# Performance work log

Hardware: AMD Instinct MI355X
Metric: run time of the kernel (lower is better)

## Reference

```python
import jax, jax.numpy as jnp
import numpy as np

EPS = 1e-6

def _complex_linear(xr, xi, wr, wi):
    # torch Linear: y = x @ W.T ; complex: (xr+i*xi)(Wr+i*Wi)
    yr = jnp.einsum('bsd,ed->bse', xr, wr) - jnp.einsum('bsd,ed->bse', xi, wi)
    yi = jnp.einsum('bsd,ed->bse', xr, wi) + jnp.einsum('bsd,ed->bse', xi, wr)
    return yr, yi

def setup_inputs() -> dict:
    key = jax.random.key(0)
    ks = jax.random.split(key, 12)
    B, S, D = 32768, 16, 64
    inp = {
        'z_real': jax.random.normal(ks[0], (B, D), jnp.float32),
        'z_imag': jax.random.normal(ks[1], (B, D), jnp.float32),
        'mem':    jax.random.normal(ks[2], (B, S, 2 * D), jnp.float32),
        'ptr':    jax.random.uniform(ks[3], (B, S), jnp.float32),
        'ctrl':   jax.random.normal(ks[4], (B, 3), jnp.float32),
        'wq_r': jax.random.normal(ks[5], (D, D), jnp.float32) / np.sqrt(D),
        'wq_i': jax.random.normal(ks[6], (D, D), jnp.float32) / np.sqrt(D),
        'wk_r': jax.random.normal(ks[7], (D, D), jnp.float32) / np.sqrt(D),
        'wk_i': jax.random.normal(ks[8], (D, D), jnp.float32) / np.sqrt(D),
        'wv_r': jax.random.normal(ks[9], (D, D), jnp.float32) / np.sqrt(D),
        'wv_i': jax.random.normal(ks[10], (D, D), jnp.float32) / np.sqrt(D),
    }
    return inp

def reference(z_real, z_imag, mem, ptr, ctrl, wq_r, wq_i, wk_r, wk_i, wv_r, wv_i):
    D = z_real.shape[-1]
    # soft push/pop/stay gates, normalized
    g = jax.nn.sigmoid(ctrl)  # (B,3)
    push, pop, stay = g[:, 0:1], g[:, 1:2], g[:, 2:3]
    total = push + pop + stay + EPS
    push, pop, stay = push / total, pop / total, stay / total
    # pointer update via rolls
    ptr_up = jnp.roll(ptr, 1, axis=1)
    ptr_down = jnp.roll(ptr, -1, axis=1)
    new_ptr = push * ptr_up + pop * ptr_down + stay * ptr  # (B,S)
    # memory write
    z_flat = jnp.concatenate([z_real, z_imag], axis=-1)  # (B,2D)
    mem_new = mem * (1.0 - push[..., None]) + push[..., None] * z_flat[:, None, :]
    mr, mi = mem_new[..., :D], mem_new[..., D:]  # (B,S,D) complex memory
    # complex attention over stack slots
    qr, qi = _complex_linear(mr, mi, wq_r, wq_i)
    kr, ki = _complex_linear(mr, mi, wk_r, wk_i)
    vr, vi = _complex_linear(mr, mi, wv_r, wv_i)
    q_flat = jnp.concatenate([qr, qi], axis=-1)  # (B,S,2D)
    k_flat = jnp.concatenate([kr, ki], axis=-1)
    scale = D ** (-0.5)
    scores = jnp.einsum('bse,bte->bst', q_flat, k_flat) * scale  # (B,S,S)
    attn = jax.nn.softmax(scores, axis=-1)
    ar = jnp.einsum('bst,btd->bsd', attn, vr)
    ai = jnp.einsum('bst,btd->bsd', attn, vi)
    att_flat = jnp.concatenate([ar, ai], axis=-1)  # (B,S,2D)
    # pointer-weighted read
    read_flat = (att_flat * new_ptr[..., None]).sum(axis=1)  # (B,2D)
    z_read_r, z_read_i = read_flat[:, :D], read_flat[:, D:]
    active_slots = (new_ptr > 0.1).astype(jnp.float32).sum(axis=1).mean()
    return (z_read_r, z_read_i, mem_new, new_ptr, active_slots)
```

## Files before the change

kernel.cpp:

```cpp
#include <hip/hip_runtime.h>


typedef __bf16 bf16x8 __attribute__((ext_vector_type(8)));
typedef float  f32x4  __attribute__((ext_vector_type(4)));

#define B_TOT   32768
#define GRID_WG 512
#define NWAVES  4096
#define BPW     8

__device__ __forceinline__ unsigned short f2bf(float x) {
  __bf16 h = (__bf16)x;
  return __builtin_bit_cast(unsigned short, h);
}
__device__ __forceinline__ float sigm(float x) { return 1.0f / (1.0f + expf(-x)); }

__global__ void ems_zero(unsigned int* c) { if (threadIdx.x == 0) *c = 0u; }

__global__ void ems_fin(const unsigned int* __restrict__ c, float* __restrict__ out) {
  if (threadIdx.x == 0) out[0] = (float)(*c) * (1.0f / 32768.0f);
}

__global__ void __launch_bounds__(128)
ems_mt(const float* __restrict__ wqr, const float* __restrict__ wqi,
       const float* __restrict__ wkr, const float* __restrict__ wki,
       unsigned short* __restrict__ mt)
{
  __shared__ float sK[128];
  const int e2 = (int)blockIdx.x;
  const int e  = (int)threadIdx.x;
  float kv;
  if (e < 64) kv = (e2 < 64) ? wkr[e*64 + e2]      : -wki[e*64 + (e2-64)];
  else        kv = (e2 < 64) ? wki[(e-64)*64 + e2] :  wkr[(e-64)*64 + (e2-64)];
  sK[e] = kv;
  __syncthreads();
  float acc = 0.0f;
  #pragma unroll 8
  for (int Ep = 0; Ep < 64; ++Ep) {
    float q = (e < 64) ? wqr[Ep*64 + e] : -wqi[Ep*64 + (e-64)];
    acc += q * sK[Ep];
  }
  #pragma unroll 8
  for (int Ep = 0; Ep < 64; ++Ep) {
    float q = (e < 64) ? wqi[Ep*64 + e] : wqr[Ep*64 + (e-64)];
    acc += q * sK[64 + Ep];
  }
  mt[e2*128 + e] = f2bf(acc);
}

__global__ void __launch_bounds__(512, 4)
ems_main(const float* __restrict__ z_real, const float* __restrict__ z_imag,
         const float* __restrict__ mem,    const float* __restrict__ ptrv,
         const float* __restrict__ ctrl,
         const float* __restrict__ wvr,    const float* __restrict__ wvi,
         const unsigned short* __restrict__ mt,
         float* __restrict__ out_zr, float* __restrict__ out_zi,
         float* __restrict__ out_mem, float* __restrict__ out_ptr,
         unsigned int* __restrict__ ws_cnt)
{
  __shared__ __align__(16) unsigned short lds[40960];

  const int tid = (int)threadIdx.x;

  for (int idx = tid; idx < 16384; idx += 512) {
    int e2 = idx >> 7, e = idx & 127;
    lds[(e2 << 7) + ((((e >> 3) ^ (e2 & 15))) << 3) + (e & 7)] = mt[idx];
  }
  #pragma unroll
  for (int m = 0; m < 2; ++m) {
    const float* wp = m ? wvi : wvr;
    for (int idx = tid; idx < 4096; idx += 512) {
      int e = idx >> 6, d = idx & 63;
      lds[16384 + (m << 12) + (e << 6) + (((d >> 3) ^ (e & 7)) << 3) + (d & 7)] = f2bf(wp[idx]);
    }
  }
  __syncthreads();

  const int lane = tid & 63;
  const int wv   = tid >> 6;
  const int c    = lane & 15;
  const int g    = lane >> 4;

  unsigned short* SY = &lds[24576 + (wv << 11)];

  const float4* mem4 = (const float4*)mem;
  const float4* zr4  = (const float4*)z_real;
  const float4* zi4  = (const float4*)z_imag;
  float4* omem4 = (float4*)out_mem;

  unsigned int active_acc = 0u;
  const int b0 = (int)blockIdx.x * 8 + wv;

  for (int it = 0; it < BPW; ++it) {
    const int b = b0 + it * NWAVES;

    float4 cm[8], cz[8];
    #pragma unroll
    for (int t4 = 0; t4 < 4; ++t4) {
      int i4 = b*512 + c*32 + t4*8 + g*2;
      cm[2*t4]   = mem4[i4];
      cm[2*t4+1] = mem4[i4+1];
    }
    {
      int zb = b*16 + g*2;
      cz[0] = zr4[zb];   cz[1] = zr4[zb+1];
      cz[2] = zr4[zb+8]; cz[3] = zr4[zb+9];
      cz[4] = zi4[zb];   cz[5] = zi4[zb+1];
      cz[6] = zi4[zb+8]; cz[7] = zi4[zb+9];
    }

    float pu = sigm(ctrl[b*3+0]);
    float po = sigm(ctrl[b*3+1]);
    float st = sigm(ctrl[b*3+2]);
    float tot = pu + po + st + 1e-6f;
    pu /= tot; po /= tot; st /= tot;

    float pm = ptrv[b*16 + ((c+15)&15)];
    float pp = ptrv[b*16 + ((c+ 1)&15)];
    float pc = ptrv[b*16 + c];
    float np = pu*pm + po*pp + st*pc;
    if (g == 0) out_ptr[b*16 + c] = np;
    unsigned long long ball = __ballot(np > 0.1f);
    active_acc += (unsigned int)__popcll(ball & 0xFFFFull);

    float omp = 1.0f - pu;
    bf16x8 af[4], afn[2];
    #pragma unroll
    for (int t4 = 0; t4 < 4; ++t4) {
      float4 a0 = cm[2*t4], a1 = cm[2*t4+1];
      float4 z0 = cz[2*t4], z1 = cz[2*t4+1];
      float4 r0, r1;
      r0.x = a0.x*omp + pu*z0.x;  r0.y = a0.y*omp + pu*z0.y;
      r0.z = a0.z*omp + pu*z0.z;  r0.w = a0.w*omp + pu*z0.w;
      r1.x = a1.x*omp + pu*z1.x;  r1.y = a1.y*omp + pu*z1.y;
      r1.z = a1.z*omp + pu*z1.z;  r1.w = a1.w*omp + pu*z1.w;
      int i4 = b*512 + c*32 + t4*8 + g*2;
      omem4[i4]   = r0;
      omem4[i4+1] = r1;
      af[t4][0]=(__bf16)r0.x; af[t4][1]=(__bf16)r0.y; af[t4][2]=(__bf16)r0.z; af[t4][3]=(__bf16)r0.w;
      af[t4][4]=(__bf16)r1.x; af[t4][5]=(__bf16)r1.y; af[t4][6]=(__bf16)r1.z; af[t4][7]=(__bf16)r1.w;
      if (t4 >= 2) {
        afn[t4-2][0]=(__bf16)(-r0.x); afn[t4-2][1]=(__bf16)(-r0.y);
        afn[t4-2][2]=(__bf16)(-r0.z); afn[t4-2][3]=(__bf16)(-r0.w);
        afn[t4-2][4]=(__bf16)(-r1.x); afn[t4-2][5]=(__bf16)(-r1.y);
        afn[t4-2][6]=(__bf16)(-r1.z); afn[t4-2][7]=(__bf16)(-r1.w);
      }
    }

    #pragma unroll
    for (int n2 = 0; n2 < 8; ++n2) {
      int e2 = (n2 << 4) + c;
      f32x4 acc = {0.f,0.f,0.f,0.f};
      #pragma unroll
      for (int t = 0; t < 4; ++t) {
        bf16x8 bm = *(const bf16x8*)&lds[(e2 << 7) + ((((t << 2) + g) ^ c) << 3)];
        acc = __builtin_amdgcn_mfma_f32_16x16x32_bf16(af[t], bm, acc, 0, 0, 0);
      }
      int chb = (n2 << 1) | (c >> 3);
      #pragma unroll
      for (int i = 0; i < 4; ++i) {
        int s = (g << 2) + i;
        SY[(s << 7) + ((chb ^ s) << 3) + (c & 7)] = f2bf(acc[i]);
      }
    }

    f32x4 sc = {0.f,0.f,0.f,0.f};
    #pragma unroll
    for (int t = 0; t < 4; ++t) {
      bf16x8 aq = *(const bf16x8*)&SY[(c << 7) + ((((t << 2) + g) ^ c) << 3)];
      sc = __builtin_amdgcn_mfma_f32_16x16x32_bf16(aq, af[t], sc, 0, 0, 0);
    }
    float a4[4];
    #pragma unroll
    for (int i = 0; i < 4; ++i) {
      float s0 = sc[i] * 0.125f;
      float mx = s0;
      mx = fmaxf(mx, __shfl_xor(mx, 1, 64));
      mx = fmaxf(mx, __shfl_xor(mx, 2, 64));
      mx = fmaxf(mx, __shfl_xor(mx, 4, 64));
      mx = fmaxf(mx, __shfl_xor(mx, 8, 64));
      float ex = expf(s0 - mx);
      float sm = ex;
      sm += __shfl_xor(sm, 1, 64);
      sm += __shfl_xor(sm, 2, 64);
      sm += __shfl_xor(sm, 4, 64);
      sm += __shfl_xor(sm, 8, 64);
      a4[i] = ex / sm;
    }

    float npi[4];
    #pragma unroll
    for (int i = 0; i < 4; ++i) npi[i] = __shfl(np, (g << 2) + i, 64);
    float pw = a4[0]*npi[0] + a4[1]*npi[1] + a4[2]*npi[2] + a4[3]*npi[3];
    pw += __shfl_xor(pw, 16, 64);
    pw += __shfl_xor(pw, 32, 64);
    float w4[4];
    #pragma unroll
    for (int i = 0; i < 4; ++i) w4[i] = __shfl(pw, (g << 2) + i, 64);

    #pragma unroll
    for (int n = 0; n < 4; ++n) {
      int e = (n << 4) + c, e7 = e & 7, eb = 16384 + (e << 6);
      f32x4 ar = {0.f,0.f,0.f,0.f}, ai = {0.f,0.f,0.f,0.f};
      #pragma unroll
      for (int t = 0; t < 2; ++t) {
        int ch = (((t << 2) + g) ^ e7) << 3;
        bf16x8 fr = *(const bf16x8*)&lds[eb + ch];
        bf16x8 fi = *(const bf16x8*)&lds[eb + 4096 + ch];
        ar = __builtin_amdgcn_mfma_f32_16x16x32_bf16(af[t],   fr, ar, 0,0,0);
        ai = __builtin_amdgcn_mfma_f32_16x16x32_bf16(af[t],   fi, ai, 0,0,0);
        ar = __builtin_amdgcn_mfma_f32_16x16x32_bf16(afn[t],  fi, ar, 0,0,0);
        ai = __builtin_amdgcn_mfma_f32_16x16x32_bf16(af[t+2], fr, ai, 0,0,0);
      }
      float prr = ar[0]*w4[0] + ar[1]*w4[1] + ar[2]*w4[2] + ar[3]*w4[3];
      float pri = ai[0]*w4[0] + ai[1]*w4[1] + ai[2]*w4[2] + ai[3]*w4[3];
      prr += __shfl_xor(prr, 16, 64);
      prr += __shfl_xor(prr, 32, 64);
      pri += __shfl_xor(pri, 16, 64);
      pri += __shfl_xor(pri, 32, 64);
      if (g == 0) {
        out_zr[b*64 + (n << 4) + c] = prr;
        out_zi[b*64 + (n << 4) + c] = pri;
      }
    }
  }

  if (lane == 0) atomicAdd(ws_cnt, active_acc);
}

extern "C" void kernel_launch(void* const* d_in, const int* in_sizes, int n_in,
                              void* d_out, int out_size, void* d_ws, size_t ws_size,
                              hipStream_t stream) {
  const float* z_real = (const float*)d_in[0];
  const float* z_imag = (const float*)d_in[1];
  const float* memp   = (const float*)d_in[2];
  const float* ptrv   = (const float*)d_in[3];
  const float* ctrl   = (const float*)d_in[4];
  const float* wq_r   = (const float*)d_in[5];
  const float* wq_i   = (const float*)d_in[6];
  const float* wk_r   = (const float*)d_in[7];
  const float* wk_i   = (const float*)d_in[8];
  const float* wv_r   = (const float*)d_in[9];
  const float* wv_i   = (const float*)d_in[10];

  float* out     = (float*)d_out;
  float* out_zr  = out;
  float* out_zi  = out + 2097152;
  float* out_mem = out + 4194304;
  float* out_ptr = out + 71303168;
  float* out_sc  = out + 71827456;

  unsigned int*   cnt = (unsigned int*)d_ws;
  unsigned short* mt  = (unsigned short*)((char*)d_ws + 1024);

  ems_zero<<<1, 64, 0, stream>>>(cnt);
  ems_mt<<<128, 128, 0, stream>>>(wq_r, wq_i, wk_r, wk_i, mt);
  ems_main<<<GRID_WG, 512, 0, stream>>>(z_real, z_imag, memp, ptrv, ctrl,
                                        wv_r, wv_i, mt,
                                        out_zr, out_zi, out_mem, out_ptr, cnt);
  ems_fin<<<1, 64, 0, stream>>>(cnt, out_sc);
}
```

Before: 180.6 us.

## Streamline softmax, fold zero kernel, use fast intrinsics and LDS-reduced counter

```diff
diff --git a/kernel.cpp b/kernel.cpp
--- a/kernel.cpp
+++ b/kernel.cpp
@@ -3,19 +3,22 @@
 
 typedef __bf16 bf16x8 __attribute__((ext_vector_type(8)));
 typedef float  f32x4  __attribute__((ext_vector_type(4)));
+typedef float  f4     __attribute__((ext_vector_type(4)));
 
 #define B_TOT   32768
 #define GRID_WG 512
 #define NWAVES  4096
 #define BPW     8
+#define LOG2E   1.4426950408889634f
+#define EXSC    0.18033688011112042f
 
 __device__ __forceinline__ unsigned short f2bf(float x) {
   __bf16 h = (__bf16)x;
   return __builtin_bit_cast(unsigned short, h);
 }
-__device__ __forceinline__ float sigm(float x) { return 1.0f / (1.0f + expf(-x)); }
-
-__global__ void ems_zero(unsigned int* c) { if (threadIdx.x == 0) *c = 0u; }
+__device__ __forceinline__ float rcp_f(float x) { return __builtin_amdgcn_rcpf(x); }
+__device__ __forceinline__ float ex2_f(float x) { return __builtin_amdgcn_exp2f(x); }
+__device__ __forceinline__ float sigm(float x) { return rcp_f(1.0f + ex2_f(-LOG2E * x)); }
 
 __global__ void ems_fin(const unsigned int* __restrict__ c, float* __restrict__ out) {
   if (threadIdx.x == 0) out[0] = (float)(*c) * (1.0f / 32768.0f);
@@ -24,8 +27,9 @@
 __global__ void __launch_bounds__(128)
 ems_mt(const float* __restrict__ wqr, const float* __restrict__ wqi,
        const float* __restrict__ wkr, const float* __restrict__ wki,
-       unsigned short* __restrict__ mt)
+       unsigned short* __restrict__ mt, unsigned int* __restrict__ cnt)
 {
+  if (blockIdx.x == 0 && threadIdx.x == 0) *cnt = 0u;
   __shared__ float sK[128];
   const int e2 = (int)blockIdx.x;
   const int e  = (int)threadIdx.x;
@@ -64,7 +68,7 @@
 
   for (int idx = tid; idx < 16384; idx += 512) {
     int e2 = idx >> 7, e = idx & 127;
-    lds[(e2 << 7) + ((((e >> 3) ^ (e2 & 15))) << 3) + (e & 7)] = mt[idx];
+    lds[(e2 << 7) + (((e >> 3) ^ (e2 & 15)) << 3) + (e & 7)] = mt[idx];
   }
   #pragma unroll
   for (int m = 0; m < 2; ++m) {
@@ -83,10 +87,10 @@
 
   unsigned short* SY = &lds[24576 + (wv << 11)];
 
-  const float4* mem4 = (const float4*)mem;
-  const float4* zr4  = (const float4*)z_real;
-  const float4* zi4  = (const float4*)z_imag;
-  float4* omem4 = (float4*)out_mem;
+  const f4* mem4 = (const f4*)mem;
+  const f4* zr4  = (const f4*)z_real;
+  const f4* zi4  = (const f4*)z_imag;
+  f4* omem4 = (f4*)out_mem;
 
   unsigned int active_acc = 0u;
   const int b0 = (int)blockIdx.x * 8 + wv;
@@ -94,7 +98,7 @@
   for (int it = 0; it < BPW; ++it) {
     const int b = b0 + it * NWAVES;
 
-    float4 cm[8], cz[8];
+    f4 cm[8], cz[8];
     #pragma unroll
     for (int t4 = 0; t4 < 4; ++t4) {
       int i4 = b*512 + c*32 + t4*8 + g*2;
@@ -112,8 +116,8 @@
     float pu = sigm(ctrl[b*3+0]);
     float po = sigm(ctrl[b*3+1]);
     float st = sigm(ctrl[b*3+2]);
-    float tot = pu + po + st + 1e-6f;
-    pu /= tot; po /= tot; st /= tot;
+    float rt = rcp_f(pu + po + st + 1e-6f);
+    pu *= rt; po *= rt; st *= rt;
 
     float pm = ptrv[b*16 + ((c+15)&15)];
     float pp = ptrv[b*16 + ((c+ 1)&15)];
@@ -123,27 +127,26 @@
     unsigned long long ball = __ballot(np > 0.1f);
     active_acc += (unsigned int)__popcll(ball & 0xFFFFull);
 
-    float omp = 1.0f - pu;
+    float om = 1.0f - pu;
     bf16x8 af[4], afn[2];
     #pragma unroll
     for (int t4 = 0; t4 < 4; ++t4) {
-      float4 a0 = cm[2*t4], a1 = cm[2*t4+1];
-      float4 z0 = cz[2*t4], z1 = cz[2*t4+1];
-      float4 r0, r1;
-      r0.x = a0.x*omp + pu*z0.x;  r0.y = a0.y*omp + pu*z0.y;
-      r0.z = a0.z*omp + pu*z0.z;  r0.w = a0.w*omp + pu*z0.w;
-      r1.x = a1.x*omp + pu*z1.x;  r1.y = a1.y*omp + pu*z1.y;
-      r1.z = a1.z*omp + pu*z1.z;  r1.w = a1.w*omp + pu*z1.w;
+      f4 r0 = cm[2*t4]   * om + pu * cz[2*t4];
+      f4 r1 = cm[2*t4+1] * om + pu * cz[2*t4+1];
       int i4 = b*512 + c*32 + t4*8 + g*2;
       omem4[i4]   = r0;
       omem4[i4+1] = r1;
-      af[t4][0]=(__bf16)r0.x; af[t4][1]=(__bf16)r0.y; af[t4][2]=(__bf16)r0.z; af[t4][3]=(__bf16)r0.w;
-      af[t4][4]=(__bf16)r1.x; af[t4][5]=(__bf16)r1.y; af[t4][6]=(__bf16)r1.z; af[t4][7]=(__bf16)r1.w;
+      #pragma unroll
+      for (int k = 0; k < 4; ++k) {
+        af[t4][k]   = (__bf16)r0[k];
+        af[t4][4+k] = (__bf16)r1[k];
+      }
       if (t4 >= 2) {
-        afn[t4-2][0]=(__bf16)(-r0.x); afn[t4-2][1]=(__bf16)(-r0.y);
-        afn[t4-2][2]=(__bf16)(-r0.z); afn[t4-2][3]=(__bf16)(-r0.w);
-        afn[t4-2][4]=(__bf16)(-r1.x); afn[t4-2][5]=(__bf16)(-r1.y);
-        afn[t4-2][6]=(__bf16)(-r1.z); afn[t4-2][7]=(__bf16)(-r1.w);
+        #pragma unroll
+        for (int k = 0; k < 4; ++k) {
+          afn[t4-2][k]   = (__bf16)(-r0[k]);
+          afn[t4-2][4+k] = (__bf16)(-r1[k]);
+        }
       }
     }
 
@@ -152,55 +155,45 @@
       int e2 = (n2 << 4) + c;
       f32x4 acc = {0.f,0.f,0.f,0.f};
       #pragma unroll
-      for (int t = 0; t < 4; ++t) {
-        bf16x8 bm = *(const bf16x8*)&lds[(e2 << 7) + ((((t << 2) + g) ^ c) << 3)];
-        acc = __builtin_amdgcn_mfma_f32_16x16x32_bf16(af[t], bm, acc, 0, 0, 0);
-      }
-      int chb = (n2 << 1) | (c >> 3);
-      #pragma unroll
-      for (int i = 0; i < 4; ++i) {
-        int s = (g << 2) + i;
-        SY[(s << 7) + ((chb ^ s) << 3) + (c & 7)] = f2bf(acc[i]);
-      }
+      for (int T = 0; T < 4; ++T) {
+        bf16x8 am = *(const bf16x8*)&lds[(e2 << 7) + ((((T << 2) + g) ^ c) << 3)];
+        acc = __builtin_amdgcn_mfma_f32_16x16x32_bf16(am, af[T], acc, 0, 0, 0);
+      }
+      uint2 pk;
+      pk.x = (unsigned)f2bf(acc[0]) | ((unsigned)f2bf(acc[1]) << 16);
+      pk.y = (unsigned)f2bf(acc[2]) | ((unsigned)f2bf(acc[3]) << 16);
+      *(uint2*)&SY[(c << 7) + ((((n2 << 1) + (g >> 1)) ^ c) << 3) + ((g & 1) << 2)] = pk;
     }
 
     f32x4 sc = {0.f,0.f,0.f,0.f};
     #pragma unroll
-    for (int t = 0; t < 4; ++t) {
-      bf16x8 aq = *(const bf16x8*)&SY[(c << 7) + ((((t << 2) + g) ^ c) << 3)];
-      sc = __builtin_amdgcn_mfma_f32_16x16x32_bf16(aq, af[t], sc, 0, 0, 0);
-    }
-    float a4[4];
-    #pragma unroll
-    for (int i = 0; i < 4; ++i) {
-      float s0 = sc[i] * 0.125f;
-      float mx = s0;
-      mx = fmaxf(mx, __shfl_xor(mx, 1, 64));
-      mx = fmaxf(mx, __shfl_xor(mx, 2, 64));
-      mx = fmaxf(mx, __shfl_xor(mx, 4, 64));
-      mx = fmaxf(mx, __shfl_xor(mx, 8, 64));
-      float ex = expf(s0 - mx);
-      float sm = ex;
-      sm += __shfl_xor(sm, 1, 64);
-      sm += __shfl_xor(sm, 2, 64);
-      sm += __shfl_xor(sm, 4, 64);
-      sm += __shfl_xor(sm, 8, 64);
-      a4[i] = ex / sm;
-    }
-
-    float npi[4];
-    #pragma unroll
-    for (int i = 0; i < 4; ++i) npi[i] = __shfl(np, (g << 2) + i, 64);
-    float pw = a4[0]*npi[0] + a4[1]*npi[1] + a4[2]*npi[2] + a4[3]*npi[3];
-    pw += __shfl_xor(pw, 16, 64);
-    pw += __shfl_xor(pw, 32, 64);
-    float w4[4];
-    #pragma unroll
-    for (int i = 0; i < 4; ++i) w4[i] = __shfl(pw, (g << 2) + i, 64);
+    for (int T = 0; T < 4; ++T) {
+      bf16x8 yb = *(const bf16x8*)&SY[(c << 7) + ((((T << 2) + g) ^ c) << 3)];
+      sc = __builtin_amdgcn_mfma_f32_16x16x32_bf16(af[T], yb, sc, 0, 0, 0);
+    }
+
+    float e0 = ex2_f(sc[0] * EXSC);
+    float e1 = ex2_f(sc[1] * EXSC);
+    float e2v = ex2_f(sc[2] * EXSC);
+    float e3 = ex2_f(sc[3] * EXSC);
+    float r = (e0 + e1) + (e2v + e3);
+    r += __shfl_xor(r, 16, 64);
+    r += __shfl_xor(r, 32, 64);
+    float u = np * rcp_f(r);
+    float v0 = u*e0, v1 = u*e1, v2 = u*e2v, v3 = u*e3;
+    #pragma unroll
+    for (int d = 1; d <= 8; d <<= 1) {
+      v0 += __shfl_xor(v0, d, 64);
+      v1 += __shfl_xor(v1, d, 64);
+      v2 += __shfl_xor(v2, d, 64);
+      v3 += __shfl_xor(v3, d, 64);
+    }
+    float w4[4] = { v0, v1, v2, v3 };
 
     #pragma unroll
     for (int n = 0; n < 4; ++n) {
-      int e = (n << 4) + c, e7 = e & 7, eb = 16384 + (e << 6);
+      int eb = 16384 + (((n << 4) + c) << 6);
+      int e7 = c & 7;
       f32x4 ar = {0.f,0.f,0.f,0.f}, ai = {0.f,0.f,0.f,0.f};
       #pragma unroll
       for (int t = 0; t < 2; ++t) {
@@ -218,14 +211,18 @@
       prr += __shfl_xor(prr, 32, 64);
       pri += __shfl_xor(pri, 16, 64);
       pri += __shfl_xor(pri, 32, 64);
-      if (g == 0) {
-        out_zr[b*64 + (n << 4) + c] = prr;
-        out_zi[b*64 + (n << 4) + c] = pri;
-      }
-    }
-  }
-
-  if (lane == 0) atomicAdd(ws_cnt, active_acc);
+      if (g == 0) out_zr[b*64 + (n << 4) + c] = prr;
+      if (g == 1) out_zi[b*64 + (n << 4) + c] = pri;
+    }
+  }
+
+  __syncthreads();
+  unsigned int* cnt_lds = (unsigned int*)&lds[24576];
+  if (tid == 0) *cnt_lds = 0u;
+  __syncthreads();
+  if (lane == 0) atomicAdd(cnt_lds, active_acc);
+  __syncthreads();
+  if (tid == 0) atomicAdd(ws_cnt, *cnt_lds);
 }
 
 extern "C" void kernel_launch(void* const* d_in, const int* in_sizes, int n_in,
@@ -251,12 +248,11 @@
   float* out_sc  = out + 71827456;
 
   unsigned int*   cnt = (unsigned int*)d_ws;
-  unsigned short* mt  = (unsigned short*)((char*)d_ws + 1024);
-
-  ems_zero<<<1, 64, 0, stream>>>(cnt);
-  ems_mt<<<128, 128, 0, stream>>>(wq_r, wq_i, wk_r, wk_i, mt);
+  unsigned short* mtp = (unsigned short*)((char*)d_ws + 1024);
+
+  ems_mt<<<128, 128, 0, stream>>>(wq_r, wq_i, wk_r, wk_i, mtp, cnt);
   ems_main<<<GRID_WG, 512, 0, stream>>>(z_real, z_imag, memp, ptrv, ctrl,
-                                        wv_r, wv_i, mt,
+                                        wv_r, wv_i, mtp,
                                         out_zr, out_zi, out_mem, out_ptr, cnt);
   ems_fin<<<1, 64, 0, stream>>>(cnt, out_sc);
 }
```

Measured after the change: 150.7 us. 1.2x faster.
